# Kernel tuning notes

Hardware: AMD Instinct MI355X
Metric: run time of the kernel (lower is better)

Reference implementation:

```python
import jax, jax.numpy as jnp
import numpy as np

C = 256
H = 8
D = C // H
B = 8
Q_PER = 128
KV_PER = 1024
NQ = B * Q_PER
NKV = B * KV_PER
NEG = -10000.0
MASK_EPS = 1e-6
RMS_EPS = float(np.finfo(np.float32).eps)  # torch RMSNorm default eps=None -> finfo eps


def _rms(x, w):
    return x * jax.lax.rsqrt(jnp.mean(x * x, axis=-1, keepdims=True) + RMS_EPS) * w


def _mlp(x, w1, b1, w2, b2):
    h = jax.nn.gelu(x @ w1.T + b1, approximate=False)  # torch nn.GELU is exact
    return h @ w2.T + b2


def _sdpa(qh, kh, vh, mask, scale):
    # qh [H, Nq, D], kh/vh [H, Nk, D], mask [Nq, Nk] additive
    s = jnp.einsum('hqd,hkd->hqk', qh, kh) * scale + mask[None]
    return jnp.einsum('hqk,hkd->hqd', jax.nn.softmax(s, axis=-1), vh)


def _heads(x):
    return x.reshape(-1, H, D).transpose(1, 0, 2)  # [H, N, D]


def setup_inputs() -> dict:
    key = jax.random.key(0)
    ks = jax.random.split(key, 24)
    s = 0.02
    lin = lambda k, o, i: jax.random.normal(k, (o, i), jnp.float32) * s
    inp = {
        'q': jax.random.normal(ks[0], (NQ, C), jnp.float32),
        'kv': jax.random.normal(ks[1], (NKV, C), jnp.float32),
        'cu_seqlens_q': jnp.arange(B + 1, dtype=jnp.int32) * Q_PER,
        'cu_seqlens_kv': jnp.arange(B + 1, dtype=jnp.int32) * KV_PER,
        'w_norm_kv': jnp.ones((C,), jnp.float32),
        'w_norm1': jnp.ones((C,), jnp.float32),
        'w_norm2': jnp.ones((C,), jnp.float32),
        'w_norm3': jnp.ones((C,), jnp.float32),
        'wq_c': lin(ks[2], C, C), 'wk_c': lin(ks[3], C, C), 'wv_c': lin(ks[4], C, C),
        'wo_c': lin(ks[5], C, C), 'bo_c': jnp.zeros((C,), jnp.float32),
        'wq_s': lin(ks[6], C, C), 'wkv_s': lin(ks[7], 2 * C, C),
        'wo_s': lin(ks[8], C, C), 'bo_s': jnp.zeros((C,), jnp.float32),
        'w1_mlp': lin(ks[9], 4 * C, C), 'b1_mlp': jnp.zeros((4 * C,), jnp.float32),
        'w2_mlp': lin(ks[10], C, 4 * C), 'b2_mlp': jnp.zeros((C,), jnp.float32),
        'w1_mask': lin(ks[11], C, C), 'b1_mask': jnp.zeros((C,), jnp.float32),
        'w2_mask': lin(ks[12], C, C), 'b2_mask': jnp.zeros((C,), jnp.float32),
    }
    return inp


def reference(q, kv, cu_seqlens_q, cu_seqlens_kv, w_norm_kv, w_norm1, w_norm2, w_norm3,
              wq_c, wk_c, wv_c, wo_c, bo_c, wq_s, wkv_s, wo_s, bo_s,
              w1_mlp, b1_mlp, w2_mlp, b2_mlp, w1_mask, b1_mask, w2_mask, b2_mask):
    scale = D ** (-0.5)
    nq, nkv = q.shape[0], kv.shape[0]
    # segment id per packed token from cu_seqlens
    seg_q = jnp.searchsorted(cu_seqlens_q, jnp.arange(nq), side='right') - 1
    seg_kv = jnp.searchsorted(cu_seqlens_kv, jnp.arange(nkv), side='right') - 1

    kv_n = _rms(kv, w_norm_kv)

    # mask MLP -> predicted attention mask (logits z), detached log-prob mask
    m_k = _mlp(q, w1_mask, b1_mask, w2_mask, b2_mask)          # [Nq, C]
    z = m_k @ kv_n.T                                           # [Nq, Nkv]
    p_hat = jax.nn.sigmoid(z)
    same = seg_q[:, None] == seg_kv[None, :]
    attn_mask = jnp.where(same, jnp.log(jax.lax.stop_gradient(p_hat) + MASK_EPS), NEG)

    # cross-attention (pre-norm)
    q_n = _rms(q, w_norm1)
    feat = _sdpa(_heads(q_n @ wq_c.T), _heads(kv_n @ wk_c.T), _heads(kv_n @ wv_c.T),
                 attn_mask, scale)
    feat = feat.transpose(1, 0, 2).reshape(-1, C) @ wo_c.T + bo_c
    q = q + feat

    # block-diagonal self-attention over queries
    q_n = _rms(q, w_norm2)
    kv_proj = (q_n @ wkv_s.T).reshape(-1, 2, H, D)
    self_mask = jnp.where(seg_q[:, None] == seg_q[None, :], 0.0, NEG)
    feat = _sdpa(_heads(q_n @ wq_s.T),
                 kv_proj[:, 0].transpose(1, 0, 2), kv_proj[:, 1].transpose(1, 0, 2),
                 self_mask, scale)
    feat = feat.transpose(1, 0, 2).reshape(-1, C) @ wo_s.T + bo_s
    q = q + feat

    # MLP
    q = q + _mlp(_rms(q, w_norm3), w1_mlp, b1_mlp, w2_mlp, b2_mlp)
    return q
```

## Files before the change

### kernel.cpp

```cpp
#include <hip/hip_runtime.h>
#include <math.h>


#define SCALE_ATTN 0.17677669529663687f
#define RMS_EPS 1.1920929e-07f

typedef __attribute__((ext_vector_type(8))) short bh8;
typedef __attribute__((ext_vector_type(4))) float f32x4;

__device__ __forceinline__ float bf2f(unsigned short s) {
  union { float f; unsigned u; } v; v.u = ((unsigned)s) << 16; return v.f;
}
__device__ __forceinline__ unsigned short f2bf(float f) {
  union { float f; unsigned u; } v; v.f = f;
  unsigned r = v.u + 0x7FFFu + ((v.u >> 16) & 1u);
  return (unsigned short)(r >> 16);
}
__device__ __forceinline__ unsigned pack2bf(float a, float b) {
  union { float f; unsigned u; } x, y; x.f = a; y.f = b;
  return ((x.u + 0x8000u) >> 16) | ((y.u + 0x8000u) & 0xFFFF0000u);
}
__device__ __forceinline__ float gelu_exact(float x) {
  return 0.5f * x * (1.0f + erff(x * 0.70710678118654752440f));
}

struct WP { const float* p[12]; };
__global__ __launch_bounds__(256) void k_pre(
    WP wp, unsigned short* __restrict__ wbf, unsigned short* __restrict__ w2t,
    const float* __restrict__ wn1, const float* __restrict__ wn2,
    const float* __restrict__ wn3,
    const float* __restrict__ kv, const float* __restrict__ wnkv,
    const float* __restrict__ b2m, unsigned short* __restrict__ kv_n,
    float* __restrict__ tvec, unsigned short* __restrict__ q_n,
    float* __restrict__ ssq2, float* __restrict__ ssq3) {
  int bid = blockIdx.x, tid = threadIdx.x;
  if (bid < 1408) {
    long g = ((long)bid * 256 + tid) * 4;
    const float* src; long l;
    if (g < 327680)       { src = wp.p[g >> 16]; l = g & 65535; }
    else if (g < 458752)  { src = wp.p[5];  l = g - 327680; }
    else if (g < 524288)  { src = wp.p[6];  l = g - 458752; }
    else if (g < 786432)  { src = wp.p[7];  l = g - 524288; }
    else if (g < 1048576) { src = wp.p[8];  l = g - 786432; }
    else if (g < 1114112) { src = wp.p[9];  l = g - 1048576; }
    else if (g < 1179648) { src = wp.p[10]; l = g - 1114112; }
    else                  { src = wp.p[11]; l = g - 1179648; }
    float4 v = *(const float4*)(src + l);
    if (g >= 262144 && g < 458752) {
      int k = (int)(g & 255);
      v.x *= wn2[k]; v.y *= wn2[k + 1]; v.z *= wn2[k + 2]; v.w *= wn2[k + 3];
    } else if (g >= 524288 && g < 786432) {
      int k = (int)(g & 255);
      v.x *= wn3[k]; v.y *= wn3[k + 1]; v.z *= wn3[k + 2]; v.w *= wn3[k + 3];
    }
    ushort4 o;
    o.x = f2bf(v.x); o.y = f2bf(v.y); o.z = f2bf(v.z); o.w = f2bf(v.w);
    *(ushort4*)(wbf + g) = o;
  } else if (bid < 1664) {
    int k = bid - 1408;
    w2t[(long)tid * 256 + k] = f2bf(wp.p[10][(long)k * 256 + tid]);
  } else if (bid < 3712) {
    int row = (bid - 1664) * 4 + (tid >> 6);
    int c4 = (tid & 63) * 4;
    float4 v = *(const float4*)(kv + (long)row * 256 + c4);
    float s = v.x * v.x + v.y * v.y + v.z * v.z + v.w * v.w;
#pragma unroll
    for (int off = 32; off > 0; off >>= 1) s += __shfl_xor(s, off, 64);
    float inv = rsqrtf(s * (1.0f / 256.0f) + RMS_EPS);
    float4 wn = *(const float4*)(wnkv + c4);
    float4 b2 = *(const float4*)(b2m + c4);
    float4 vn;
    vn.x = v.x * inv * wn.x; vn.y = v.y * inv * wn.y;
    vn.z = v.z * inv * wn.z; vn.w = v.w * inv * wn.w;
    ushort4 o;
    o.x = f2bf(vn.x); o.y = f2bf(vn.y); o.z = f2bf(vn.z); o.w = f2bf(vn.w);
    *(ushort4*)(kv_n + (long)row * 256 + c4) = o;
    float s2 = vn.x * b2.x + vn.y * b2.y + vn.z * b2.z + vn.w * b2.w;
#pragma unroll
    for (int off = 32; off > 0; off >>= 1) s2 += __shfl_xor(s2, off, 64);
    if ((tid & 63) == 0) tvec[row] = s2;
  } else if (bid < 3968) {
    int row = (bid - 3712) * 4 + (tid >> 6);
    int c4 = (tid & 63) * 4;
    const float* q = wp.p[11];
    float4 v = *(const float4*)(q + (long)row * 256 + c4);
    float s = v.x * v.x + v.y * v.y + v.z * v.z + v.w * v.w;
#pragma unroll
    for (int off = 32; off > 0; off >>= 1) s += __shfl_xor(s, off, 64);
    float inv = rsqrtf(s * (1.0f / 256.0f) + RMS_EPS);
    float4 wn = *(const float4*)(wn1 + c4);
    ushort4 o;
    o.x = f2bf(v.x * inv * wn.x); o.y = f2bf(v.y * inv * wn.y);
    o.z = f2bf(v.z * inv * wn.z); o.w = f2bf(v.w * inv * wn.w);
    *(ushort4*)(q_n + (long)row * 256 + c4) = o;
  } else {
    int idx = (bid - 3968) * 256 + tid;
    if (idx < 1024) ssq2[idx] = 0.f;
    else if (idx < 2048) ssq3[idx - 1024] = 0.f;
  }
}

template <int MT>
__device__ __forceinline__ void gemm_core(
    const unsigned short* __restrict__ A, const unsigned short* __restrict__ W,
    const float* bias, const float* R, const float* ssqIn, float* ssqOut,
    float* Cf, unsigned short* Cb, unsigned short* Cb2,
    int K, int lda, int ldw, int ldc, int m0, int n0, int epi) {
  int tid = threadIdx.x, w = tid >> 6, lane = tid & 63;
  int quad = lane >> 4, c = lane & 15;
  __shared__ __align__(16) unsigned short As[MT * 64][40];
  __shared__ __align__(16) unsigned short Ws[64][40];
  f32x4 acc[MT][4];
#pragma unroll
  for (int i = 0; i < MT; ++i)
#pragma unroll
    for (int j = 0; j < 4; ++j) acc[i][j] = (f32x4){0.f, 0.f, 0.f, 0.f};
  int ar = tid >> 2, ak = (tid & 3) * 8;
  for (int k0 = 0; k0 < K; k0 += 32) {
    int4 a0 = *(const int4*)(A + (long)(m0 + ar) * lda + k0 + ak);
    int4 a1;
    if (MT == 2) a1 = *(const int4*)(A + (long)(m0 + 64 + ar) * lda + k0 + ak);
    int4 wv = *(const int4*)(W + (long)(n0 + ar) * ldw + k0 + ak);
    __syncthreads();
    *(int4*)&As[ar][ak] = a0;
    if (MT == 2) *(int4*)&As[64 + ar][ak] = a1;
    *(int4*)&Ws[ar][ak] = wv;
    __syncthreads();
    bh8 af[MT];
#pragma unroll
    for (int mt = 0; mt < MT; ++mt)
      af[mt] = *(const bh8*)&As[w * (16 * MT) + mt * 16 + c][quad * 8];
#pragma unroll
    for (int nt = 0; nt < 4; ++nt) {
      bh8 bf = *(const bh8*)&Ws[nt * 16 + c][quad * 8];
#pragma unroll
      for (int mt = 0; mt < MT; ++mt)
        acc[mt][nt] =
            __builtin_amdgcn_mfma_f32_16x16x32_bf16(af[mt], bf, acc[mt][nt], 0, 0, 0);
    }
  }
  float rsum[MT][4];
#pragma unroll
  for (int mt = 0; mt < MT; ++mt)
#pragma unroll
    for (int r = 0; r < 4; ++r) rsum[mt][r] = 0.f;
#pragma unroll
  for (int mt = 0; mt < MT; ++mt)
#pragma unroll
    for (int nt = 0; nt < 4; ++nt)
#pragma unroll
      for (int r = 0; r < 4; ++r) {
        int m = m0 + w * (16 * MT) + mt * 16 + quad * 4 + r;
        int n = n0 + nt * 16 + c;
        float v = acc[mt][nt][r];
        long ci = (long)m * ldc + n;
        if (epi == 1) {
          if (bias) v += bias[n];
          Cb[ci] = f2bf(gelu_exact(v));
        } else if (epi == 5) {
          Cb[ci] = f2bf(v);
        } else if (epi == 3) {
          if (bias) v += bias[n];
          Cb[ci] = f2bf(1.0f / (1.0f + __expf(-v)) + 1e-6f);
        } else if (epi == 2) {
          if (bias) v += bias[n];
          v += R[ci];
          Cf[ci] = v;
          if (Cb2) Cb2[ci] = f2bf(v);
          rsum[mt][r] += v * v;
        } else if (epi == 6) {
          v *= rsqrtf(ssqIn[m] * (1.0f / 256.0f) + RMS_EPS);
          if (bias) v += bias[n];
          Cb[ci] = f2bf(gelu_exact(v));
        } else {
          v *= rsqrtf(ssqIn[m] * (1.0f / 256.0f) + RMS_EPS);
          Cb[ci] = f2bf(v);
        }
      }
  if (epi == 2 && ssqOut) {
#pragma unroll
    for (int mt = 0; mt < MT; ++mt)
#pragma unroll
      for (int r = 0; r < 4; ++r) {
        float s = rsum[mt][r];
        s += __shfl_xor(s, 1, 64);
        s += __shfl_xor(s, 2, 64);
        s += __shfl_xor(s, 4, 64);
        s += __shfl_xor(s, 8, 64);
        if (c == 0)
          atomicAdd(&ssqOut[m0 + w * (16 * MT) + mt * 16 + quad * 4 + r], s);
      }
  }
}

template <int MT>
__global__ __launch_bounds__(256) void k_gemm(
    const unsigned short* A, const unsigned short* W,
    const float* bias, long sBh, const float* R,
    const float* ssqIn, float* ssqOut,
    float* Cf, unsigned short* Cb, unsigned short* Cb2,
    int K, int lda, int ldw, int ldc, long sAh, long sWh, long sCh, int epi) {
  int z = blockIdx.z;
  long coff = (long)z * sCh;
  gemm_core<MT>(A + (long)z * sAh, W + (long)z * sWh,
                bias ? bias + (long)z * sBh : nullptr, R, ssqIn, ssqOut,
                Cf ? Cf + coff : nullptr, Cb ? Cb + coff : nullptr, Cb2,
                K, lda, ldw, ldc, blockIdx.y * (MT * 64), blockIdx.x * 64, epi);
}

struct G4 {
  const unsigned short* A; const unsigned short* W;
  const float* bias; float* Cf; unsigned short* Cb;
  int K, lda, ldw, ldc, epi, nx, blkStart;
};
struct G4x { G4 g[4]; };
__global__ __launch_bounds__(256) void k_gemm4(G4x d) {
  int z = blockIdx.x;
  int i = 3;
  while (i > 0 && z < d.g[i].blkStart) --i;
  const G4& g = d.g[i];
  int local = z - g.blkStart;
  int by = local / g.nx, bx = local - by * g.nx;
  gemm_core<2>(g.A, g.W, g.bias, nullptr, nullptr, nullptr,
               g.Cf, g.Cb, nullptr, g.K, g.lda, g.ldw, g.ldc,
               by * 128, bx * 64, g.epi);
}

template <int MODE>
__global__ __launch_bounds__(256) void k_flash(
    const unsigned short* __restrict__ Qg, int ldq,
    const unsigned short* __restrict__ KVg, int ldkv, int kvRows,
    int kOff, int vOff, const unsigned short* __restrict__ maskp,
    unsigned short* __restrict__ feat,
    float* __restrict__ partL, float* __restrict__ partO) {
  int split = blockIdx.x, bh = blockIdx.y;
  int b = bh >> 3, h = bh & 7, j0 = split * 128;
  int tid = threadIdx.x;
  int w = tid >> 6, lane = tid & 63, c = lane & 15, quad = lane >> 4;
  __shared__ __align__(16) unsigned short Ks[128][40];
  __shared__ __align__(16) unsigned short Vt[32][136];
  __shared__ __align__(16) unsigned short Pt[128][136];
  const unsigned short* Qz = Qg + (long)(b * 128) * ldq + h * 32;
  const unsigned short* Kz = KVg + ((long)b * kvRows + j0) * ldkv + kOff + h * 32;
  const unsigned short* Vz = KVg + ((long)b * kvRows + j0) * ldkv + vOff + h * 32;
  bh8 Bq[2];
#pragma unroll
  for (int nt = 0; nt < 2; ++nt)
    Bq[nt] = *(const bh8*)(Qz + (long)(w * 32 + nt * 16 + c) * ldq + quad * 8);
  {
    int row = tid >> 2, part = tid & 3;
#pragma unroll
    for (int v = 0; v < 2; ++v) {
      int r2 = row + v * 64;
      *(int4*)&Ks[r2][part * 8] = *(const int4*)(Kz + (long)r2 * ldkv + part * 8);
      int4 vv = *(const int4*)(Vz + (long)r2 * ldkv + part * 8);
      unsigned short tmp[8];
      *(int4*)tmp = vv;
#pragma unroll
      for (int i = 0; i < 8; ++i) Vt[part * 8 + i][r2] = tmp[i];
    }
  }
  __syncthreads();
  f32x4 S[8][2];
#pragma unroll
  for (int mt = 0; mt < 8; ++mt)
#pragma unroll
    for (int nt = 0; nt < 2; ++nt) S[mt][nt] = (f32x4){0.f, 0.f, 0.f, 0.f};
#pragma unroll
  for (int mt = 0; mt < 8; ++mt) {
    bh8 aK = *(const bh8*)&Ks[mt * 16 + c][quad * 8];
    S[mt][0] = __builtin_amdgcn_mfma_f32_16x16x32_bf16(aK, Bq[0], S[mt][0], 0, 0, 0);
    S[mt][1] = __builtin_amdgcn_mfma_f32_16x16x32_bf16(aK, Bq[1], S[mt][1], 0, 0, 0);
  }
  float L[2];
#pragma unroll
  for (int nt = 0; nt < 2; ++nt) {
    if (MODE == 0) {
      const unsigned short* mrow =
          maskp + ((long)(b * 128 + w * 32 + nt * 16 + c)) * 1024 + j0;
#pragma unroll
      for (int mt = 0; mt < 8; ++mt) {
        uint2 mp = *(const uint2*)(mrow + mt * 16 + quad * 4);
        S[mt][nt][0] = __expf(S[mt][nt][0] * SCALE_ATTN) * bf2f((unsigned short)mp.x);
        S[mt][nt][1] = __expf(S[mt][nt][1] * SCALE_ATTN) * bf2f((unsigned short)(mp.x >> 16));
        S[mt][nt][2] = __expf(S[mt][nt][2] * SCALE_ATTN) * bf2f((unsigned short)mp.y);
        S[mt][nt][3] = __expf(S[mt][nt][3] * SCALE_ATTN) * bf2f((unsigned short)(mp.y >> 16));
      }
    } else {
#pragma unroll
      for (int mt = 0; mt < 8; ++mt)
#pragma unroll
        for (int r = 0; r < 4; ++r)
          S[mt][nt][r] = __expf(S[mt][nt][r] * SCALE_ATTN);
    }
    float rs = 0.f;
#pragma unroll
    for (int mt = 0; mt < 8; ++mt)
#pragma unroll
      for (int r = 0; r < 4; ++r) rs += S[mt][nt][r];
    rs += __shfl_xor(rs, 16, 64);
    rs += __shfl_xor(rs, 32, 64);
    L[nt] = rs;
  }
#pragma unroll
  for (int mt = 0; mt < 8; ++mt)
#pragma unroll
    for (int nt = 0; nt < 2; ++nt) {
      uint2 pk;
      pk.x = pack2bf(S[mt][nt][0], S[mt][nt][1]);
      pk.y = pack2bf(S[mt][nt][2], S[mt][nt][3]);
      *(uint2*)&Pt[w * 32 + nt * 16 + c][mt * 16 + quad * 4] = pk;
    }
  __syncthreads();
  f32x4 acc[2][2];
#pragma unroll
  for (int i = 0; i < 2; ++i)
#pragma unroll
    for (int j = 0; j < 2; ++j) acc[i][j] = (f32x4){0.f, 0.f, 0.f, 0.f};
#pragma unroll
  for (int ks = 0; ks < 4; ++ks) {
    bh8 aP0 = *(const bh8*)&Pt[w * 32 + c][ks * 32 + quad * 8];
    bh8 aP1 = *(const bh8*)&Pt[w * 32 + 16 + c][ks * 32 + quad * 8];
    bh8 bV0 = *(const bh8*)&Vt[c][ks * 32 + quad * 8];
    bh8 bV1 = *(const bh8*)&Vt[16 + c][ks * 32 + quad * 8];
    acc[0][0] = __builtin_amdgcn_mfma_f32_16x16x32_bf16(aP0, bV0, acc[0][0], 0, 0, 0);
    acc[0][1] = __builtin_amdgcn_mfma_f32_16x16x32_bf16(aP0, bV1, acc[0][1], 0, 0, 0);
    acc[1][0] = __builtin_amdgcn_mfma_f32_16x16x32_bf16(aP1, bV0, acc[1][0], 0, 0, 0);
    acc[1][1] = __builtin_amdgcn_mfma_f32_16x16x32_bf16(aP1, bV1, acc[1][1], 0, 0, 0);
  }
  if (MODE == 0) {
    if (quad == 0) {
#pragma unroll
      for (int nt = 0; nt < 2; ++nt)
        partL[((long)(bh * 128 + w * 32 + nt * 16 + c)) * 8 + split] = L[nt];
    }
#pragma unroll
    for (int mt = 0; mt < 2; ++mt)
#pragma unroll
      for (int ct = 0; ct < 2; ++ct)
#pragma unroll
        for (int r = 0; r < 4; ++r) {
          int q = w * 32 + mt * 16 + quad * 4 + r;
          partO[(((long)(bh * 128 + q)) * 8 + split) * 32 + ct * 16 + c] =
              acc[mt][ct][r];
        }
  } else {
    unsigned short* Oz = feat + (long)(b * 128) * 256 + h * 32;
#pragma unroll
    for (int mt = 0; mt < 2; ++mt)
#pragma unroll
      for (int r = 0; r < 4; ++r) {
        float linv = 1.0f / __shfl(L[mt], quad * 4 + r, 64);
        int q = w * 32 + mt * 16 + quad * 4 + r;
        Oz[(long)q * 256 + c] = f2bf(acc[mt][0][r] * linv);
        Oz[(long)q * 256 + 16 + c] = f2bf(acc[mt][1][r] * linv);
      }
  }
}

__global__ __launch_bounds__(256) void k_combine(
    const float* __restrict__ partL, const float* __restrict__ partO,
    unsigned short* __restrict__ feat) {
  int task = blockIdx.x * 256 + threadIdx.x;
  int bh = task >> 7, qq = task & 127, b = bh >> 3, h = bh & 7;
  const float* pl = partL + (long)task * 8;
  float L = 0.f;
#pragma unroll
  for (int s = 0; s < 8; ++s) L += pl[s];
  float inv = 1.0f / L;
  float o[32] = {0.f};
  const float* po = partO + (long)task * 256;
#pragma unroll
  for (int s = 0; s < 8; ++s)
#pragma unroll
    for (int d4 = 0; d4 < 8; ++d4) {
      float4 v = *(const float4*)(po + s * 32 + d4 * 4);
      o[d4 * 4 + 0] += v.x; o[d4 * 4 + 1] += v.y;
      o[d4 * 4 + 2] += v.z; o[d4 * 4 + 3] += v.w;
    }
  unsigned short* op = feat + (long)(b * 128 + qq) * 256 + h * 32;
#pragma unroll
  for (int d4 = 0; d4 < 8; ++d4) {
    ushort4 w4;
    w4.x = f2bf(o[d4 * 4 + 0] * inv); w4.y = f2bf(o[d4 * 4 + 1] * inv);
    w4.z = f2bf(o[d4 * 4 + 2] * inv); w4.w = f2bf(o[d4 * 4 + 3] * inv);
    *(ushort4*)(op + d4 * 4) = w4;
  }
}

extern "C" void kernel_launch(void* const* d_in, const int* in_sizes, int n_in,
                              void* d_out, int out_size, void* d_ws, size_t ws_size,
                              hipStream_t stream) {
  const float* q        = (const float*)d_in[0];
  const float* kv       = (const float*)d_in[1];
  const float* w_norm_kv = (const float*)d_in[4];
  const float* w_norm1  = (const float*)d_in[5];
  const float* w_norm2  = (const float*)d_in[6];
  const float* w_norm3  = (const float*)d_in[7];
  const float* bo_c     = (const float*)d_in[12];
  const float* bo_s     = (const float*)d_in[16];
  const float* b1_mlp   = (const float*)d_in[18];
  const float* b2_mlp   = (const float*)d_in[20];
  const float* b1_mask  = (const float*)d_in[22];
  const float* b2_mask  = (const float*)d_in[24];
  float* out = (float*)d_out;

  unsigned char* W8 = (unsigned char*)d_ws;
  unsigned short* wbf    = (unsigned short*)(W8 + 0);
  unsigned short* w2t    = (unsigned short*)(W8 + 2883584);
  unsigned short* kv_n   = (unsigned short*)(W8 + 3014656);
  unsigned short* q_n    = (unsigned short*)(W8 + 7208960);
  unsigned short* mh     = (unsigned short*)(W8 + 7733248);
  unsigned short* kvw    = (unsigned short*)(W8 + 8257536);
  unsigned short* maskp  = (unsigned short*)(W8 + 12451840);
  float*          tvec   = (float*)(W8 + 14548992);
  unsigned short* Qc     = (unsigned short*)(W8 + 14581760);
  unsigned short* KVc    = (unsigned short*)(W8 + 15106048);
  unsigned short* QKVs   = (unsigned short*)(W8 + 23494656);
  unsigned short* feat   = (unsigned short*)(W8 + 25067520);
  unsigned short* out1_bf = (unsigned short*)(W8 + 25591808);
  unsigned short* out2_bf = (unsigned short*)(W8 + 26116096);
  float*          ssq2   = (float*)(W8 + 26640384);
  float*          ssq3   = (float*)(W8 + 26644480);
  float*          partL  = (float*)(W8 + 26648832);
  float*          partO  = (float*)(W8 + 26910976);
  unsigned short* hid    = (unsigned short*)(W8 + 35299584);

  unsigned short* wq_c_bf   = wbf;
  unsigned short* wkv_c_bf  = wbf + 65536;
  unsigned short* wo_c_bf   = wbf + 196608;
  unsigned short* wqkv_s_bf = wbf + 262144;
  unsigned short* wo_s_bf   = wbf + 458752;
  unsigned short* w1_mlp_bf = wbf + 524288;
  unsigned short* w2_mlp_bf = wbf + 786432;
  unsigned short* w1_mask_bf = wbf + 1048576;
  unsigned short* q_bf      = wbf + 1179648;

  WP wp;
  wp.p[0] = (const float*)d_in[8];  wp.p[1] = (const float*)d_in[9];
  wp.p[2] = (const float*)d_in[10]; wp.p[3] = (const float*)d_in[11];
  wp.p[4] = (const float*)d_in[13]; wp.p[5] = (const float*)d_in[14];
  wp.p[6] = (const float*)d_in[15]; wp.p[7] = (const float*)d_in[17];
  wp.p[8] = (const float*)d_in[19]; wp.p[9] = (const float*)d_in[21];
  wp.p[10] = (const float*)d_in[23]; wp.p[11] = q;
  k_pre<<<3976, 256, 0, stream>>>(wp, wbf, w2t, w_norm1, w_norm2, w_norm3,
                                  kv, w_norm_kv, b2_mask, kv_n, tvec, q_n,
                                  ssq2, ssq3);

  G4x d;
  d.g[0] = {q_bf, w1_mask_bf, b1_mask, nullptr, mh, 256, 256, 256, 256, 1, 4, 0};
  d.g[1] = {q_n, wq_c_bf, nullptr, nullptr, Qc, 256, 256, 256, 256, 5, 4, 32};
  d.g[2] = {kv_n, wkv_c_bf, nullptr, nullptr, KVc, 256, 256, 256, 512, 5, 8, 64};
  d.g[3] = {kv_n, w2t, nullptr, nullptr, kvw, 256, 256, 256, 256, 5, 4, 576};
  k_gemm4<<<832, 256, 0, stream>>>(d);

  k_gemm<1><<<dim3(16, 2, 8), 256, 0, stream>>>(mh, kvw, tvec, 1024, nullptr,
      nullptr, nullptr, nullptr, maskp, nullptr,
      256, 256, 256, 1024, 128L * 256, 1024L * 256, 128L * 1024, 3);

  k_flash<0><<<dim3(8, 64), 256, 0, stream>>>(Qc, 256, KVc, 512, 1024, 0, 256,
                                              maskp, nullptr, partL, partO);
  k_combine<<<32, 256, 0, stream>>>(partL, partO, feat);
  k_gemm<1><<<dim3(4, 16, 1), 256, 0, stream>>>(feat, wo_c_bf, bo_c, 0, q,
      nullptr, ssq2, out, nullptr, out1_bf, 256, 256, 256, 256, 0, 0, 0, 2);

  k_gemm<1><<<dim3(12, 16, 1), 256, 0, stream>>>(out1_bf, wqkv_s_bf, nullptr, 0,
      nullptr, ssq2, nullptr, nullptr, QKVs, nullptr,
      256, 256, 256, 768, 0, 0, 0, 7);
  k_flash<1><<<dim3(1, 64), 256, 0, stream>>>(QKVs, 768, QKVs, 768, 128, 256,
                                              512, nullptr, feat, nullptr,
                                              nullptr);
  k_gemm<1><<<dim3(4, 16, 1), 256, 0, stream>>>(feat, wo_s_bf, bo_s, 0, out,
      nullptr, ssq3, out, nullptr, out2_bf, 256, 256, 256, 256, 0, 0, 0, 2);

  k_gemm<1><<<dim3(16, 16, 1), 256, 0, stream>>>(out2_bf, w1_mlp_bf, b1_mlp, 0,
      nullptr, ssq3, nullptr, nullptr, hid, nullptr,
      256, 256, 256, 1024, 0, 0, 0, 6);
  k_gemm<1><<<dim3(4, 16, 1), 256, 0, stream>>>(hid, w2_mlp_bf, b2_mlp, 0, out,
      nullptr, nullptr, out, nullptr, nullptr,
      1024, 1024, 1024, 256, 0, 0, 0, 2);
}
```

Before: 227.5 us.

## Double-buffer GEMM tiles, fuse flash combine into output GEMM, tile w2 transpose

The GEMM core now double-buffers its shared-memory A/W tiles, issuing global loads for the next K-slice while MFMAs run on the current one. K becomes a compile-time template parameter so the loop fully unrolls, and one barrier per iteration is removed. The separate split-KV combine kernel is folded into a new GEMM that reduces the partial outputs while building its A tile, which removes a launch and a round trip through global memory for feat. The w2 transpose in the prep kernel now uses a shared-memory tiled transpose instead of strided scalar writes. The cost is doubled LDS use per block, more registers from the unrolled loops, and combine work that is recomputed for each of the four N-blocks.

```diff
diff --git a/kernel.cpp b/kernel.cpp
--- a/kernel.cpp
+++ b/kernel.cpp
@@ -56,11 +56,29 @@
     ushort4 o;
     o.x = f2bf(v.x); o.y = f2bf(v.y); o.z = f2bf(v.z); o.w = f2bf(v.w);
     *(ushort4*)(wbf + g) = o;
-  } else if (bid < 1664) {
-    int k = bid - 1408;
-    w2t[(long)tid * 256 + k] = f2bf(wp.p[10][(long)k * 256 + tid]);
-  } else if (bid < 3712) {
-    int row = (bid - 1664) * 4 + (tid >> 6);
+  } else if (bid < 1424) {
+    __shared__ float Ts[64][65];
+    int t = bid - 1408, ti = t >> 2, tj = t & 3;
+    const float* w2src = wp.p[10];
+    int rr = tid >> 2;
+#pragma unroll
+    for (int j = 0; j < 4; ++j) {
+      int cc = (tid & 3) * 16 + j * 4;
+      float4 v = *(const float4*)(w2src + (long)(ti * 64 + rr) * 256 + tj * 64 + cc);
+      Ts[rr][cc] = v.x; Ts[rr][cc + 1] = v.y;
+      Ts[rr][cc + 2] = v.z; Ts[rr][cc + 3] = v.w;
+    }
+    __syncthreads();
+#pragma unroll
+    for (int j = 0; j < 4; ++j) {
+      int kk = (tid & 3) * 16 + j * 4;
+      ushort4 o;
+      o.x = f2bf(Ts[kk][rr]); o.y = f2bf(Ts[kk + 1][rr]);
+      o.z = f2bf(Ts[kk + 2][rr]); o.w = f2bf(Ts[kk + 3][rr]);
+      *(ushort4*)(w2t + (long)(tj * 64 + rr) * 256 + ti * 64 + kk) = o;
+    }
+  } else if (bid < 3472) {
+    int row = (bid - 1424) * 4 + (tid >> 6);
     int c4 = (tid & 63) * 4;
     float4 v = *(const float4*)(kv + (long)row * 256 + c4);
     float s = v.x * v.x + v.y * v.y + v.z * v.z + v.w * v.w;
@@ -79,8 +97,8 @@
 #pragma unroll
     for (int off = 32; off > 0; off >>= 1) s2 += __shfl_xor(s2, off, 64);
     if ((tid & 63) == 0) tvec[row] = s2;
-  } else if (bid < 3968) {
-    int row = (bid - 3712) * 4 + (tid >> 6);
+  } else if (bid < 3728) {
+    int row = (bid - 3472) * 4 + (tid >> 6);
     int c4 = (tid & 63) * 4;
     const float* q = wp.p[11];
     float4 v = *(const float4*)(q + (long)row * 256 + c4);
@@ -94,49 +112,66 @@
     o.z = f2bf(v.z * inv * wn.z); o.w = f2bf(v.w * inv * wn.w);
     *(ushort4*)(q_n + (long)row * 256 + c4) = o;
   } else {
-    int idx = (bid - 3968) * 256 + tid;
+    int idx = (bid - 3728) * 256 + tid;
     if (idx < 1024) ssq2[idx] = 0.f;
     else if (idx < 2048) ssq3[idx - 1024] = 0.f;
   }
 }
 
-template <int MT>
+template <int MT, int KS>
 __device__ __forceinline__ void gemm_core(
     const unsigned short* __restrict__ A, const unsigned short* __restrict__ W,
     const float* bias, const float* R, const float* ssqIn, float* ssqOut,
     float* Cf, unsigned short* Cb, unsigned short* Cb2,
-    int K, int lda, int ldw, int ldc, int m0, int n0, int epi) {
+    int lda, int ldw, int ldc, int m0, int n0, int epi) {
   int tid = threadIdx.x, w = tid >> 6, lane = tid & 63;
   int quad = lane >> 4, c = lane & 15;
-  __shared__ __align__(16) unsigned short As[MT * 64][40];
-  __shared__ __align__(16) unsigned short Ws[64][40];
+  __shared__ __align__(16) unsigned short As[2][MT * 64][40];
+  __shared__ __align__(16) unsigned short Ws[2][64][40];
   f32x4 acc[MT][4];
 #pragma unroll
   for (int i = 0; i < MT; ++i)
 #pragma unroll
     for (int j = 0; j < 4; ++j) acc[i][j] = (f32x4){0.f, 0.f, 0.f, 0.f};
   int ar = tid >> 2, ak = (tid & 3) * 8;
-  for (int k0 = 0; k0 < K; k0 += 32) {
-    int4 a0 = *(const int4*)(A + (long)(m0 + ar) * lda + k0 + ak);
+  {
+    int4 a0 = *(const int4*)(A + (long)(m0 + ar) * lda + ak);
     int4 a1;
-    if (MT == 2) a1 = *(const int4*)(A + (long)(m0 + 64 + ar) * lda + k0 + ak);
-    int4 wv = *(const int4*)(W + (long)(n0 + ar) * ldw + k0 + ak);
-    __syncthreads();
-    *(int4*)&As[ar][ak] = a0;
-    if (MT == 2) *(int4*)&As[64 + ar][ak] = a1;
-    *(int4*)&Ws[ar][ak] = wv;
-    __syncthreads();
+    if (MT == 2) a1 = *(const int4*)(A + (long)(m0 + 64 + ar) * lda + ak);
+    int4 wv = *(const int4*)(W + (long)(n0 + ar) * ldw + ak);
+    *(int4*)&As[0][ar][ak] = a0;
+    if (MT == 2) *(int4*)&As[0][64 + ar][ak] = a1;
+    *(int4*)&Ws[0][ar][ak] = wv;
+  }
+  __syncthreads();
+#pragma unroll
+  for (int i = 0; i < KS; ++i) {
+    int cur = i & 1, nxt = cur ^ 1;
+    int4 na0, na1, nwv;
+    if (i + 1 < KS) {
+      int k0 = (i + 1) * 32;
+      na0 = *(const int4*)(A + (long)(m0 + ar) * lda + k0 + ak);
+      if (MT == 2)
+        na1 = *(const int4*)(A + (long)(m0 + 64 + ar) * lda + k0 + ak);
+      nwv = *(const int4*)(W + (long)(n0 + ar) * ldw + k0 + ak);
+    }
     bh8 af[MT];
 #pragma unroll
     for (int mt = 0; mt < MT; ++mt)
-      af[mt] = *(const bh8*)&As[w * (16 * MT) + mt * 16 + c][quad * 8];
+      af[mt] = *(const bh8*)&As[cur][w * (16 * MT) + mt * 16 + c][quad * 8];
 #pragma unroll
     for (int nt = 0; nt < 4; ++nt) {
-      bh8 bf = *(const bh8*)&Ws[nt * 16 + c][quad * 8];
+      bh8 bf = *(const bh8*)&Ws[cur][nt * 16 + c][quad * 8];
 #pragma unroll
       for (int mt = 0; mt < MT; ++mt)
         acc[mt][nt] =
             __builtin_amdgcn_mfma_f32_16x16x32_bf16(af[mt], bf, acc[mt][nt], 0, 0, 0);
+    }
+    if (i + 1 < KS) {
+      *(int4*)&As[nxt][ar][ak] = na0;
+      if (MT == 2) *(int4*)&As[nxt][64 + ar][ak] = na1;
+      *(int4*)&Ws[nxt][ar][ak] = nwv;
+      __syncthreads();
     }
   }
   float rsum[MT][4];
@@ -193,25 +228,25 @@
   }
 }
 
-template <int MT>
+template <int MT, int KS>
 __global__ __launch_bounds__(256) void k_gemm(
     const unsigned short* A, const unsigned short* W,
     const float* bias, long sBh, const float* R,
     const float* ssqIn, float* ssqOut,
     float* Cf, unsigned short* Cb, unsigned short* Cb2,
-    int K, int lda, int ldw, int ldc, long sAh, long sWh, long sCh, int epi) {
+    int lda, int ldw, int ldc, long sAh, long sWh, long sCh, int epi) {
   int z = blockIdx.z;
   long coff = (long)z * sCh;
-  gemm_core<MT>(A + (long)z * sAh, W + (long)z * sWh,
-                bias ? bias + (long)z * sBh : nullptr, R, ssqIn, ssqOut,
-                Cf ? Cf + coff : nullptr, Cb ? Cb + coff : nullptr, Cb2,
-                K, lda, ldw, ldc, blockIdx.y * (MT * 64), blockIdx.x * 64, epi);
+  gemm_core<MT, KS>(A + (long)z * sAh, W + (long)z * sWh,
+                    bias ? bias + (long)z * sBh : nullptr, R, ssqIn, ssqOut,
+                    Cf ? Cf + coff : nullptr, Cb ? Cb + coff : nullptr, Cb2,
+                    lda, ldw, ldc, blockIdx.y * (MT * 64), blockIdx.x * 64, epi);
 }
 
 struct G4 {
   const unsigned short* A; const unsigned short* W;
   const float* bias; float* Cf; unsigned short* Cb;
-  int K, lda, ldw, ldc, epi, nx, blkStart;
+  int lda, ldw, ldc, epi, nx, blkStart;
 };
 struct G4x { G4 g[4]; };
 __global__ __launch_bounds__(256) void k_gemm4(G4x d) {
@@ -221,9 +256,109 @@
   const G4& g = d.g[i];
   int local = z - g.blkStart;
   int by = local / g.nx, bx = local - by * g.nx;
-  gemm_core<2>(g.A, g.W, g.bias, nullptr, nullptr, nullptr,
-               g.Cf, g.Cb, nullptr, g.K, g.lda, g.ldw, g.ldc,
-               by * 128, bx * 64, g.epi);
+  gemm_core<2, 8>(g.A, g.W, g.bias, nullptr, nullptr, nullptr,
+                  g.Cf, g.Cb, nullptr, g.lda, g.ldw, g.ldc,
+                  by * 128, bx * 64, g.epi);
+}
+
+__global__ __launch_bounds__(256) void k_gemm_cmb(
+    const float* __restrict__ partL, const float* __restrict__ partO,
+    const unsigned short* __restrict__ W, const float* __restrict__ bias,
+    const float* __restrict__ R, float* __restrict__ ssqOut,
+    float* __restrict__ Cf, unsigned short* __restrict__ Cb2) {
+  int m0 = blockIdx.y * 64, n0 = blockIdx.x * 64;
+  int tid = threadIdx.x, w = tid >> 6, lane = tid & 63;
+  int quad = lane >> 4, c = lane & 15;
+  __shared__ __align__(16) unsigned short As[2][64][40];
+  __shared__ __align__(16) unsigned short Ws[2][64][40];
+  __shared__ float Linv[64][8];
+  int ar = tid >> 2, ak = (tid & 3) * 8;
+  int b = m0 >> 7, q0 = m0 & 127;
+  {
+#pragma unroll
+    for (int t = 0; t < 2; ++t) {
+      int e = tid * 2 + t;
+      int rr = e >> 3, hh = e & 7;
+      const float* pl = partL + ((long)((b * 8 + hh) * 128 + q0 + rr)) * 8;
+      float Ls = 0.f;
+#pragma unroll
+      for (int s = 0; s < 8; ++s) Ls += pl[s];
+      Linv[rr][hh] = 1.0f / Ls;
+    }
+  }
+  __syncthreads();
+  auto computeA = [&](int i, uint4& pk) {
+    const float* po =
+        partO + (((long)((b * 8 + i) * 128 + q0 + ar)) * 8) * 32 + ak;
+    float o0 = 0, o1 = 0, o2 = 0, o3 = 0, o4 = 0, o5 = 0, o6 = 0, o7 = 0;
+#pragma unroll
+    for (int s = 0; s < 8; ++s) {
+      float4 u = *(const float4*)(po + s * 32);
+      float4 v = *(const float4*)(po + s * 32 + 4);
+      o0 += u.x; o1 += u.y; o2 += u.z; o3 += u.w;
+      o4 += v.x; o5 += v.y; o6 += v.z; o7 += v.w;
+    }
+    float inv = Linv[ar][i];
+    pk.x = pack2bf(o0 * inv, o1 * inv);
+    pk.y = pack2bf(o2 * inv, o3 * inv);
+    pk.z = pack2bf(o4 * inv, o5 * inv);
+    pk.w = pack2bf(o6 * inv, o7 * inv);
+  };
+  f32x4 acc[4];
+#pragma unroll
+  for (int j = 0; j < 4; ++j) acc[j] = (f32x4){0.f, 0.f, 0.f, 0.f};
+  {
+    uint4 pk;
+    computeA(0, pk);
+    int4 wv = *(const int4*)(W + (long)(n0 + ar) * 256 + ak);
+    *(uint4*)&As[0][ar][ak] = pk;
+    *(int4*)&Ws[0][ar][ak] = wv;
+  }
+  __syncthreads();
+#pragma unroll
+  for (int i = 0; i < 8; ++i) {
+    int cur = i & 1, nxt = cur ^ 1;
+    uint4 npk;
+    int4 nwv;
+    if (i + 1 < 8) {
+      computeA(i + 1, npk);
+      nwv = *(const int4*)(W + (long)(n0 + ar) * 256 + (i + 1) * 32 + ak);
+    }
+    bh8 af = *(const bh8*)&As[cur][w * 16 + c][quad * 8];
+#pragma unroll
+    for (int nt = 0; nt < 4; ++nt) {
+      bh8 bf = *(const bh8*)&Ws[cur][nt * 16 + c][quad * 8];
+      acc[nt] = __builtin_amdgcn_mfma_f32_16x16x32_bf16(af, bf, acc[nt], 0, 0, 0);
+    }
+    if (i + 1 < 8) {
+      *(uint4*)&As[nxt][ar][ak] = npk;
+      *(int4*)&Ws[nxt][ar][ak] = nwv;
+      __syncthreads();
+    }
+  }
+  float rsum[4] = {0.f, 0.f, 0.f, 0.f};
+#pragma unroll
+  for (int nt = 0; nt < 4; ++nt)
+#pragma unroll
+    for (int r = 0; r < 4; ++r) {
+      int m = m0 + w * 16 + quad * 4 + r;
+      int n = n0 + nt * 16 + c;
+      float v = acc[nt][r] + bias[n];
+      long ci = (long)m * 256 + n;
+      v += R[ci];
+      Cf[ci] = v;
+      Cb2[ci] = f2bf(v);
+      rsum[r] += v * v;
+    }
+#pragma unroll
+  for (int r = 0; r < 4; ++r) {
+    float s = rsum[r];
+    s += __shfl_xor(s, 1, 64);
+    s += __shfl_xor(s, 2, 64);
+    s += __shfl_xor(s, 4, 64);
+    s += __shfl_xor(s, 8, 64);
+    if (c == 0) atomicAdd(&ssqOut[m0 + w * 16 + quad * 4 + r], s);
+  }
 }
 
 template <int MODE>
@@ -355,36 +490,6 @@
         Oz[(long)q * 256 + c] = f2bf(acc[mt][0][r] * linv);
         Oz[(long)q * 256 + 16 + c] = f2bf(acc[mt][1][r] * linv);
       }
-  }
-}
-
-__global__ __launch_bounds__(256) void k_combine(
-    const float* __restrict__ partL, const float* __restrict__ partO,
-    unsigned short* __restrict__ feat) {
-  int task = blockIdx.x * 256 + threadIdx.x;
-  int bh = task >> 7, qq = task & 127, b = bh >> 3, h = bh & 7;
-  const float* pl = partL + (long)task * 8;
-  float L = 0.f;
-#pragma unroll
-  for (int s = 0; s < 8; ++s) L += pl[s];
-  float inv = 1.0f / L;
-  float o[32] = {0.f};
-  const float* po = partO + (long)task * 256;
-#pragma unroll
-  for (int s = 0; s < 8; ++s)
-#pragma unroll
-    for (int d4 = 0; d4 < 8; ++d4) {
-      float4 v = *(const float4*)(po + s * 32 + d4 * 4);
-      o[d4 * 4 + 0] += v.x; o[d4 * 4 + 1] += v.y;
-      o[d4 * 4 + 2] += v.z; o[d4 * 4 + 3] += v.w;
-    }
-  unsigned short* op = feat + (long)(b * 128 + qq) * 256 + h * 32;
-#pragma unroll
-  for (int d4 = 0; d4 < 8; ++d4) {
-    ushort4 w4;
-    w4.x = f2bf(o[d4 * 4 + 0] * inv); w4.y = f2bf(o[d4 * 4 + 1] * inv);
-    w4.z = f2bf(o[d4 * 4 + 2] * inv); w4.w = f2bf(o[d4 * 4 + 3] * inv);
-    *(ushort4*)(op + d4 * 4) = w4;
   }
 }
 
@@ -443,40 +548,39 @@
   wp.p[6] = (const float*)d_in[15]; wp.p[7] = (const float*)d_in[17];
   wp.p[8] = (const float*)d_in[19]; wp.p[9] = (const float*)d_in[21];
   wp.p[10] = (const float*)d_in[23]; wp.p[11] = q;
-  k_pre<<<3976, 256, 0, stream>>>(wp, wbf, w2t, w_norm1, w_norm2, w_norm3,
+  k_pre<<<3736, 256, 0, stream>>>(wp, wbf, w2t, w_norm1, w_norm2, w_norm3,
                                   kv, w_norm_kv, b2_mask, kv_n, tvec, q_n,
                                   ssq2, ssq3);
 
   G4x d;
-  d.g[0] = {q_bf, w1_mask_bf, b1_mask, nullptr, mh, 256, 256, 256, 256, 1, 4, 0};
-  d.g[1] = {q_n, wq_c_bf, nullptr, nullptr, Qc, 256, 256, 256, 256, 5, 4, 32};
-  d.g[2] = {kv_n, wkv_c_bf, nullptr, nullptr, KVc, 256, 256, 256, 512, 5, 8, 64};
-  d.g[3] = {kv_n, w2t, nullptr, nullptr, kvw, 256, 256, 256, 256, 5, 4, 576};
+  d.g[0] = {q_bf, w1_mask_bf, b1_mask, nullptr, mh, 256, 256, 256, 1, 4, 0};
+  d.g[1] = {q_n, wq_c_bf, nullptr, nullptr, Qc, 256, 256, 256, 5, 4, 32};
+  d.g[2] = {kv_n, wkv_c_bf, nullptr, nullptr, KVc, 256, 256, 512, 5, 8, 64};
+  d.g[3] = {kv_n, w2t, nullptr, nullptr, kvw, 256, 256, 256, 5, 4, 576};
   k_gemm4<<<832, 256, 0, stream>>>(d);
 
-  k_gemm<1><<<dim3(16, 2, 8), 256, 0, stream>>>(mh, kvw, tvec, 1024, nullptr,
+  k_gemm<1, 8><<<dim3(16, 2, 8), 256, 0, stream>>>(mh, kvw, tvec, 1024, nullptr,
       nullptr, nullptr, nullptr, maskp, nullptr,
-      256, 256, 256, 1024, 128L * 256, 1024L * 256, 128L * 1024, 3);
+      256, 256, 1024, 128L * 256, 1024L * 256, 128L * 1024, 3);
 
   k_flash<0><<<dim3(8, 64), 256, 0, stream>>>(Qc, 256, KVc, 512, 1024, 0, 256,
                                               maskp, nullptr, partL, partO);
-  k_combine<<<32, 256, 0, stream>>>(partL, partO, feat);
-  k_gemm<1><<<dim3(4, 16, 1), 256, 0, stream>>>(feat, wo_c_bf, bo_c, 0, q,
-      nullptr, ssq2, out, nullptr, out1_bf, 256, 256, 256, 256, 0, 0, 0, 2);
-
-  k_gemm<1><<<dim3(12, 16, 1), 256, 0, stream>>>(out1_bf, wqkv_s_bf, nullptr, 0,
-      nullptr, ssq2, nullptr, nullptr, QKVs, nullptr,
-      256, 256, 256, 768, 0, 0, 0, 7);
+  k_gemm_cmb<<<dim3(4, 16), 256, 0, stream>>>(partL, partO, wo_c_bf, bo_c, q,
+                                              ssq2, out, out1_bf);
+
+  k_gemm<1, 8><<<dim3(12, 16, 1), 256, 0, stream>>>(out1_bf, wqkv_s_bf, nullptr,
+      0, nullptr, ssq2, nullptr, nullptr, QKVs, nullptr,
+      256, 256, 768, 0, 0, 0, 7);
   k_flash<1><<<dim3(1, 64), 256, 0, stream>>>(QKVs, 768, QKVs, 768, 128, 256,
                                               512, nullptr, feat, nullptr,
                                               nullptr);
-  k_gemm<1><<<dim3(4, 16, 1), 256, 0, stream>>>(feat, wo_s_bf, bo_s, 0, out,
-      nullptr, ssq3, out, nullptr, out2_bf, 256, 256, 256, 256, 0, 0, 0, 2);
-
-  k_gemm<1><<<dim3(16, 16, 1), 256, 0, stream>>>(out2_bf, w1_mlp_bf, b1_mlp, 0,
-      nullptr, ssq3, nullptr, nullptr, hid, nullptr,
-      256, 256, 256, 1024, 0, 0, 0, 6);
-  k_gemm<1><<<dim3(4, 16, 1), 256, 0, stream>>>(hid, w2_mlp_bf, b2_mlp, 0, out,
-      nullptr, nullptr, out, nullptr, nullptr,
-      1024, 1024, 1024, 256, 0, 0, 0, 2);
-}
+  k_gemm<1, 8><<<dim3(4, 16, 1), 256, 0, stream>>>(feat, wo_s_bf, bo_s, 0, out,
+      nullptr, ssq3, out, nullptr, out2_bf, 256, 256, 256, 0, 0, 0, 2);
+
+  k_gemm<1, 8><<<dim3(16, 16, 1), 256, 0, stream>>>(out2_bf, w1_mlp_bf, b1_mlp,
+      0, nullptr, ssq3, nullptr, nullptr, hid, nullptr,
+      256, 256, 1024, 0, 0, 0, 6);
+  k_gemm<1, 32><<<dim3(4, 16, 1), 256, 0, stream>>>(hid, w2_mlp_bf, b2_mlp, 0,
+      out, nullptr, nullptr, out, nullptr, nullptr,
+      1024, 1024, 256, 0, 0, 0, 2);
+}
```

New measurement: 213.5 us. 6.2% less time.
